# Kernel tuning notes

Measured on AMD Instinct MI355X. Metric: run time of the kernel, lower is better.

The kernel has to match this reference:

```python
import jax, jax.numpy as jnp
import numpy as np

K = 20          # neighbour_num
EMB = 512       # emb_dims
EPS = 1e-12     # guards sqrt grad at self-neighbor zero distance


def setup_inputs() -> dict:
    key = jax.random.key(0)
    ks = jax.random.split(key, 6)
    B, D, N = 8, 3, 4096
    C_in = 2 * D + K  # 26 = 6 + neighbour_num
    def xavier(k, o, c):
        return jax.random.normal(k, (o, c), jnp.float32) * jnp.sqrt(2.0 / (o + c))
    return {
        "x":  jax.random.normal(ks[0], (B, D, N), jnp.float32),
        "w1": xavier(ks[1], 64, C_in),
        "w2": xavier(ks[2], 64, 64),
        "w3": xavier(ks[3], 128, 64),
        "w4": xavier(ks[4], 256, 128),
        "w5": xavier(ks[5], EMB, 512),
    }


def _graph_feature(x):
    # x: (B, D, N). Returns (B, 2D+K, N, K).
    B, D, N = x.shape
    xt = jnp.swapaxes(x, 1, 2)                      # (B, N, D)
    sq = jnp.sum(x * x, axis=1)                     # (B, N)
    # pairwise = -||xi - xj||^2 ; topk picks nearest neighbors (incl. self)
    pair = 2.0 * jnp.einsum('bdn,bdm->bnm', x, x) - sq[:, :, None] - sq[:, None, :]
    idx = jax.lax.top_k(pair, K)[1]                 # (B, N, K) int32
    nbr = xt[jnp.arange(B)[:, None, None], idx]     # (B, N, K, D) gather
    xc = jnp.broadcast_to(xt[:, :, None, :], (B, N, K, D))
    dist = jnp.sqrt(jnp.sum((nbr - xc) ** 2, axis=-1) + EPS)   # (B, N, K)
    distr = jnp.broadcast_to(dist[:, :, None, :], (B, N, K, K))
    feat = jnp.concatenate([xc, nbr, distr], axis=-1)          # (B, N, K, 2D+K)
    return jnp.transpose(feat, (0, 3, 1, 2))        # (B, 2D+K, N, K)


def _conv1x1(h, w):
    # h: (B, C, N, K), w: (O, C)  -> (B, O, N, K)
    return jnp.einsum('bcnk,oc->bonk', h, w)


def reference(x, w1, w2, w3, w4, w5):
    h = _graph_feature(x)                           # (B, 26, N, K)
    h = jax.nn.relu(_conv1x1(h, w1)); x1 = h.max(axis=-1)   # (B, 64, N)
    h = jax.nn.relu(_conv1x1(h, w2)); x2 = h.max(axis=-1)   # (B, 64, N)
    h = jax.nn.relu(_conv1x1(h, w3)); x3 = h.max(axis=-1)   # (B, 128, N)
    h = jax.nn.relu(_conv1x1(h, w4)); x4 = h.max(axis=-1)   # (B, 256, N)
    cat = jnp.concatenate([x1, x2, x3, x4], axis=1)          # (B, 512, N)
    out = jax.nn.relu(jnp.einsum('bcn,oc->bon', cat, w5))    # (B, EMB, N)
    return out
```

## Files before the change

### kernel.cpp

```cpp
#include <hip/hip_runtime.h>
#include <cstdint>
#include <cstddef>

#define NB   8
#define NPTS 4096
#define KNN  20
#define P    4
#define QPW  4
#define WPB  8

typedef __attribute__((ext_vector_type(8))) short    short8;
typedef __attribute__((ext_vector_type(4))) float    floatx4;

__device__ __forceinline__ uint16_t f2bf(float f) {
    uint32_t u = __float_as_uint(f);
    uint32_t r = (u + 0x7FFFu + ((u >> 16) & 1u)) >> 16;
    return (uint16_t)r;
}

__device__ __forceinline__ uint32_t cvtpk_bf16(float lo, float hi) {
    uint32_t r;
    asm("v_cvt_pk_bf16_f32 %0, %1, %2" : "=v"(r) : "v"(lo), "v"(hi));
    return r;
}

#define NEGINF __int_as_float((int)0xFF800000)

__device__ __forceinline__ float rfl_f32(float v) {
    return __uint_as_float((uint32_t)__builtin_amdgcn_readfirstlane(__float_as_uint(v)));
}

template <int CTRL>
__device__ __forceinline__ float dpp_maxf(float v) {
    int o = __builtin_amdgcn_update_dpp(__float_as_int(v), __float_as_int(v),
                                        CTRL, 0xF, 0xF, false);
    return fmaxf(v, __int_as_float(o));
}
__device__ __forceinline__ float wave_max_f32(float v) {
    v = dpp_maxf<0x111>(v);
    v = dpp_maxf<0x112>(v);
    v = dpp_maxf<0x114>(v);
    v = dpp_maxf<0x118>(v);
    v = dpp_maxf<0x142>(v);
    v = dpp_maxf<0x143>(v);
    return __int_as_float(__builtin_amdgcn_readlane(__float_as_int(v), 63));
}

__global__ __launch_bounds__(512, 6) void topk_kernel(
    const float* __restrict__ x,
    int*   __restrict__ idx_out,
    float* __restrict__ dist_out)
{
    const int t = threadIdx.x;
    const int wave = t >> 6, l = t & 63;
    const int b = blockIdx.y;

    __shared__ float xs[NPTS], ys[NPTS], zs[NPTS];
    {
        const float* xb = x + (size_t)b * 3 * NPTS;
        for (int i = t; i < NPTS; i += WPB * 64) {
            xs[i] = xb[i];
            ys[i] = xb[NPTS + i];
            zs[i] = xb[2 * NPTS + i];
        }
    }
    __syncthreads();

    const int nbase = (blockIdx.x * WPB + wave) * QPW;

    float xn0[QPW], xn1[QPW], xn2[QPW], sqn[QPW];
    float V0[QPW], V1[QPW], V2[QPW];
    int   J0[QPW], J1[QPW], J2[QPW];
    int   my_m[QPW];

    #pragma unroll
    for (int p = 0; p < QPW; ++p) {
        const int n = nbase + p;
        const float qx = xs[n], qy = ys[n], qz = zs[n];
        xn0[p] = rfl_f32(qx); xn1[p] = rfl_f32(qy); xn2[p] = rfl_f32(qz);
        sqn[p] = rfl_f32(fmaf(qz, qz, fmaf(qy, qy, qx * qx)));
        V0[p] = NEGINF; V1[p] = NEGINF; V2[p] = NEGINF;
        J0[p] = 0; J1[p] = 0; J2[p] = 0;
        my_m[p] = 0;
    }

    #pragma unroll 2
    for (int j = 0; j < 64; ++j) {
        const float px = xs[j * 64 + l], py = ys[j * 64 + l], pz = zs[j * 64 + l];
        const float sqm = fmaf(pz, pz, fmaf(py, py, px * px));
        #pragma unroll
        for (int p = 0; p < QPW; ++p) {
            const float dot = fmaf(xn2[p], pz, fmaf(xn1[p], py, xn0[p] * px));
            const float s = fmaf(2.0f, dot, -sqn[p]) - sqm;
            const bool c0 = s > V0[p], c1 = s > V1[p], c2 = s > V2[p];
            const float nV2 = __builtin_amdgcn_fmed3f(V1[p], V2[p], s);
            const float nV1 = __builtin_amdgcn_fmed3f(V0[p], V1[p], s);
            V0[p] = fmaxf(V0[p], s);
            V1[p] = nV1; V2[p] = nV2;
            const int tA = c1 ? J1[p] : j;
            J2[p] = c2 ? tA : J2[p];
            const int tB = c0 ? J0[p] : j;
            J1[p] = c1 ? tB : J1[p];
            J0[p] = c0 ? j : J0[p];
        }
    }

    for (int k = 0; k < KNN; ++k) {
        #pragma unroll
        for (int p = 0; p < QPW; ++p) {
            if (V0[p] == NEGINF) {
                unsigned long long cons = 0ull;
                for (int i = 0; i < k; ++i) {
                    const int mw = __builtin_amdgcn_readlane(my_m[p], i);
                    if ((mw & 63) == l) cons |= 1ull << (mw >> 6);
                }
                V1[p] = NEGINF; V2[p] = NEGINF;
                for (int j = 0; j < 64; ++j) {
                    const float px = xs[j * 64 + l], py = ys[j * 64 + l], pz = zs[j * 64 + l];
                    const float sqm = fmaf(pz, pz, fmaf(py, py, px * px));
                    const float dot = fmaf(xn2[p], pz, fmaf(xn1[p], py, xn0[p] * px));
                    float s = fmaf(2.0f, dot, -sqn[p]) - sqm;
                    if ((cons >> j) & 1ull) s = NEGINF;
                    const bool c0 = s > V0[p], c1 = s > V1[p], c2 = s > V2[p];
                    const float nV2 = __builtin_amdgcn_fmed3f(V1[p], V2[p], s);
                    const float nV1 = __builtin_amdgcn_fmed3f(V0[p], V1[p], s);
                    V0[p] = fmaxf(V0[p], s);
                    V1[p] = nV1; V2[p] = nV2;
                    const int tA = c1 ? J1[p] : j;
                    J2[p] = c2 ? tA : J2[p];
                    const int tB = c0 ? J0[p] : j;
                    J1[p] = c1 ? tB : J1[p];
                    J0[p] = c0 ? j : J0[p];
                }
            }
        }
        float wv[QPW];
        #pragma unroll
        for (int p = 0; p < QPW; ++p) wv[p] = wave_max_f32(V0[p]);
        #pragma unroll
        for (int p = 0; p < QPW; ++p) {
            const unsigned long long own = __ballot(V0[p] == wv[p]);
            const int owner = (int)__builtin_ctzll(own);
            const int jwin  = __builtin_amdgcn_readlane(J0[p], owner);
            const int m     = jwin * 64 + owner;
            if (l == k) my_m[p] = m;
            if (l == owner) {
                V0[p] = V1[p]; V1[p] = V2[p]; V2[p] = NEGINF;
                J0[p] = J1[p]; J1[p] = J2[p];
            }
        }
    }

    #pragma unroll
    for (int p = 0; p < QPW; ++p) {
        if (l < KNN) {
            const int n = nbase + p;
            const int m = my_m[p];
            const float d0 = xs[m] - xn0[p], d1 = ys[m] - xn1[p], d2 = zs[m] - xn2[p];
            const float dist = sqrtf(((d0 * d0 + d1 * d1) + d2 * d2) + 1e-12f);
            const size_t base = ((size_t)b * NPTS + n) * KNN + l;
            idx_out[base]  = m;
            dist_out[base] = dist;
        }
    }
}

__global__ __launch_bounds__(256) void prep_all(
    const float* __restrict__ w1, const float* __restrict__ w2,
    const float* __restrict__ w3, const float* __restrict__ w4,
    const float* __restrict__ w5,
    uint16_t* __restrict__ wf1, uint16_t* __restrict__ wf2,
    uint16_t* __restrict__ wf3, uint16_t* __restrict__ wf4,
    uint16_t* __restrict__ w5b)
{
    int blk = blockIdx.x;
    const int t = threadIdx.x;
    if (blk < 1024) {
        const int i = blk * 256 + t;
        w5b[i] = f2bf(w5[i]);
        return;
    }
    blk -= 1024;
    const float* w; uint16_t* frag; int C, NT, KT, base;
    if (blk < 1)       { w = w1; frag = wf1; C = 26;  NT = 4;  KT = 1; base = blk; }
    else if (blk < 3)  { w = w2; frag = wf2; C = 64;  NT = 4;  KT = 2; base = blk - 1; }
    else if (blk < 7)  { w = w3; frag = wf3; C = 64;  NT = 8;  KT = 2; base = blk - 3; }
    else               { w = w4; frag = wf4; C = 128; NT = 16; KT = 4; base = blk - 7; }
    const int i = base * 256 + t;
    if (i >= NT * KT * 64) return;
    const int lane = i & 63;
    const int kt   = (i >> 6) % KT;
    const int nt   = (i >> 6) / KT;
    const int n    = nt * 16 + (lane & 15);
    const int c0   = kt * 32 + (lane >> 4) * 8;
    uint16_t o[8];
    #pragma unroll
    for (int j = 0; j < 8; ++j) {
        const int c = c0 + j;
        o[j] = (c < C) ? f2bf(w[(size_t)n * C + c]) : (uint16_t)0;
    }
    uint16_t* dst = frag + (size_t)i * 8;
    #pragma unroll
    for (int j = 0; j < 8; ++j) dst[j] = o[j];
}

template <int NT_TOT, int KT, int IN_STRIDE, int OUT_STRIDE>
__device__ __forceinline__ void mfma_layer(const uint16_t* __restrict__ in,
                                           uint16_t* __restrict__ out,
                                           const uint16_t* __restrict__ wf,
                                           int wave, int lane) {
    constexpr int NT_W = NT_TOT / 4;
    const int col = lane & 15, quad = lane >> 4;
    short8 bfrag[NT_W][KT];
    #pragma unroll
    for (int ni = 0; ni < NT_W; ++ni)
        #pragma unroll
        for (int k = 0; k < KT; ++k)
            bfrag[ni][k] = *(const short8*)(wf +
                ((size_t)((wave * NT_W + ni) * KT + k) * 64 + lane) * 8);
    #pragma unroll
    for (int mt = 0; mt < 5; ++mt) {
        short8 af[KT];
        #pragma unroll
        for (int k = 0; k < KT; ++k)
            af[k] = *(const short8*)(in + (mt * 16 + col) * IN_STRIDE + k * 32 + quad * 8);
        #pragma unroll
        for (int ni = 0; ni < NT_W; ++ni) {
            floatx4 acc = {0.f, 0.f, 0.f, 0.f};
            #pragma unroll
            for (int k = 0; k < KT; ++k)
                acc = __builtin_amdgcn_mfma_f32_16x16x32_bf16(af[k], bfrag[ni][k], acc, 0, 0, 0);
            const int nt = wave * NT_W + ni;
            const int rowb = mt * 16 + quad * 4;
            const uint32_t pk01 = cvtpk_bf16(fmaxf(acc[0], 0.f), fmaxf(acc[1], 0.f));
            const uint32_t pk23 = cvtpk_bf16(fmaxf(acc[2], 0.f), fmaxf(acc[3], 0.f));
            out[(rowb + 0) * OUT_STRIDE + nt * 16 + col] = (uint16_t)pk01;
            out[(rowb + 1) * OUT_STRIDE + nt * 16 + col] = (uint16_t)(pk01 >> 16);
            out[(rowb + 2) * OUT_STRIDE + nt * 16 + col] = (uint16_t)pk23;
            out[(rowb + 3) * OUT_STRIDE + nt * 16 + col] = (uint16_t)(pk23 >> 16);
        }
    }
}

template <int O, int STRIDE>
__device__ __forceinline__ void maxk(const uint16_t* __restrict__ h,
                                     uint16_t* __restrict__ cat_ws, int catoff,
                                     int t, int b, int n0) {
    constexpr int G = O / 8;
    if (t < P * G) {
        const int p = t / G, g = t % G;
        uint16_t mx[8];
        #pragma unroll
        for (int j = 0; j < 8; ++j) mx[j] = 0;
        for (int k = 0; k < KNN; ++k) {
            const uint16_t* row = h + (p * KNN + k) * STRIDE + g * 8;
            #pragma unroll
            for (int j = 0; j < 8; ++j) mx[j] = row[j] > mx[j] ? row[j] : mx[j];
        }
        uint16_t* dst = cat_ws + ((size_t)b * NPTS + n0 + p) * 512 + catoff + g * 8;
        *(short8*)dst = *(const short8*)mx;
    }
}

__global__ __launch_bounds__(256) void fused_mlp_mfma(
    const float* __restrict__ x,
    const int*   __restrict__ idx_ws,
    const float* __restrict__ dist_ws,
    const uint16_t* __restrict__ wf1,
    const uint16_t* __restrict__ wf2,
    const uint16_t* __restrict__ wf3,
    const uint16_t* __restrict__ wf4,
    uint16_t* __restrict__ cat_ws)
{
    const int n0 = blockIdx.x * P, b = blockIdx.y, t = threadIdx.x;
    const int wave = t >> 6, lane = t & 63;

    __shared__ __align__(16) uint16_t bufA[12800];
    __shared__ __align__(16) uint16_t bufB[10880];

    for (int i = t; i < 1600; i += 256) ((uint32_t*)bufA)[i] = 0;
    __syncthreads();
    {
        const float* xb = x + (size_t)b * 3 * NPTS;
        if (t < P * KNN) {
            const int p = t / KNN, k = t % KNN;
            const int n = n0 + p;
            const size_t base = ((size_t)b * NPTS + n) * KNN + k;
            const int   m = idx_ws[base];
            const float d = dist_ws[base];
            uint16_t* fr = bufA + t * 40;
            fr[0] = f2bf(xb[n]);        fr[1] = f2bf(xb[NPTS + n]);
            fr[2] = f2bf(xb[2 * NPTS + n]);
            fr[3] = f2bf(xb[m]);        fr[4] = f2bf(xb[NPTS + m]);
            fr[5] = f2bf(xb[2 * NPTS + m]);
            const uint16_t db = f2bf(d);
            #pragma unroll
            for (int j = 0; j < KNN; ++j) bufA[(p * KNN + j) * 40 + 6 + k] = db;
        }
    }
    __syncthreads();

    mfma_layer<4, 1, 40, 72>(bufA, bufB, wf1, wave, lane);
    __syncthreads();

    maxk<64, 72>(bufB, cat_ws, 0, t, b, n0);
    mfma_layer<4, 2, 72, 72>(bufB, bufA, wf2, wave, lane);
    __syncthreads();

    maxk<64, 72>(bufA, cat_ws, 64, t, b, n0);
    mfma_layer<8, 2, 72, 136>(bufA, bufB, wf3, wave, lane);
    __syncthreads();

    maxk<128, 136>(bufB, cat_ws, 128, t, b, n0);
    {
        float* slab = (float*)bufA + wave * 1600;
        const int col = lane & 15, quad = lane >> 4;
        #pragma unroll
        for (int ni = 0; ni < 4; ++ni) {
            const int nt = wave * 4 + ni;
            short8 bfrag[4];
            #pragma unroll
            for (int k = 0; k < 4; ++k)
                bfrag[k] = *(const short8*)(wf4 + ((size_t)(nt * 4 + k) * 64 + lane) * 8);
            #pragma unroll
            for (int mt = 0; mt < 5; ++mt) {
                floatx4 acc = {0.f, 0.f, 0.f, 0.f};
                #pragma unroll
                for (int k = 0; k < 4; ++k) {
                    const short8 af = *(const short8*)(bufB + (mt * 16 + col) * 136
                                                           + k * 32 + quad * 8);
                    acc = __builtin_amdgcn_mfma_f32_16x16x32_bf16(af, bfrag[k], acc, 0, 0, 0);
                }
                #pragma unroll
                for (int r = 0; r < 4; ++r)
                    slab[(mt * 16 + quad * 4 + r) * 20 + col] = fmaxf(acc[r], 0.f);
            }
            const int p = lane >> 4, grp = (lane >> 2) & 3, kq = lane & 3;
            floatx4 mx = {0.f, 0.f, 0.f, 0.f};
            #pragma unroll
            for (int i = 0; i < 5; ++i) {
                const floatx4 v = *(const floatx4*)&slab[(p * KNN + kq * 5 + i) * 20 + grp * 4];
                mx[0] = fmaxf(mx[0], v[0]); mx[1] = fmaxf(mx[1], v[1]);
                mx[2] = fmaxf(mx[2], v[2]); mx[3] = fmaxf(mx[3], v[3]);
            }
            #pragma unroll
            for (int r = 0; r < 4; ++r) {
                mx[r] = fmaxf(mx[r], __shfl_xor(mx[r], 1));
                mx[r] = fmaxf(mx[r], __shfl_xor(mx[r], 2));
            }
            if (kq == 0) {
                const uint32_t p01 = cvtpk_bf16(mx[0], mx[1]);
                const uint32_t p23 = cvtpk_bf16(mx[2], mx[3]);
                uint32_t* dst = (uint32_t*)(cat_ws + ((size_t)b * NPTS + n0 + p) * 512
                              + 256 + nt * 16 + grp * 4);
                dst[0] = p01; dst[1] = p23;
            }
        }
    }
}

__global__ __launch_bounds__(256) void final_gemm_mfma(
    const uint16_t* __restrict__ w5b,
    const uint16_t* __restrict__ cat,
    float* __restrict__ out)
{
    const int b  = blockIdx.z;
    const int o0 = blockIdx.y * 64;
    const int n0 = blockIdx.x * 128;
    const int t  = threadIdx.x;
    const int wave = t >> 6, lane = t & 63;
    const int col = lane & 15, quad = lane >> 4;

    __shared__ __align__(16) uint16_t As[64 * 72];
    __shared__ __align__(16) uint16_t Bs[128 * 72];

    floatx4 acc[8];
    #pragma unroll
    for (int i = 0; i < 8; ++i) acc[i] = (floatx4){0.f, 0.f, 0.f, 0.f};

    const size_t arow_base = (size_t)o0 * 512;
    const size_t brow_base = ((size_t)b * NPTS + n0) * 512;

    for (int kc = 0; kc < 512; kc += 64) {
        #pragma unroll
        for (int i = 0; i < 2; ++i) {
            const int idx = t + i * 256;
            const int row = idx >> 3;
            const int k8  = (idx & 7) * 8;
            *(short8*)&As[row * 72 + k8] =
                *(const short8*)&w5b[arow_base + (size_t)row * 512 + kc + k8];
        }
        #pragma unroll
        for (int i = 0; i < 4; ++i) {
            const int idx = t + i * 256;
            const int row = idx >> 3;
            const int k8  = (idx & 7) * 8;
            *(short8*)&Bs[row * 72 + k8] =
                *(const short8*)&cat[brow_base + (size_t)row * 512 + kc + k8];
        }
        __syncthreads();
        #pragma unroll
        for (int kt = 0; kt < 2; ++kt) {
            const short8 af = *(const short8*)&As[(wave * 16 + col) * 72 + kt * 32 + quad * 8];
            #pragma unroll
            for (int ns = 0; ns < 8; ++ns) {
                const short8 bf = *(const short8*)&Bs[(ns * 16 + col) * 72 + kt * 32 + quad * 8];
                acc[ns] = __builtin_amdgcn_mfma_f32_16x16x32_bf16(af, bf, acc[ns], 0, 0, 0);
            }
        }
        __syncthreads();
    }

    #pragma unroll
    for (int ns = 0; ns < 8; ++ns) {
        #pragma unroll
        for (int r = 0; r < 4; ++r) {
            out[((size_t)b * 512 + o0 + wave * 16 + quad * 4 + r) * NPTS
                + n0 + ns * 16 + col] = fmaxf(acc[ns][r], 0.f);
        }
    }
}

extern "C" void kernel_launch(void* const* d_in, const int* in_sizes, int n_in,
                              void* d_out, int out_size, void* d_ws, size_t ws_size,
                              hipStream_t stream) {
    const float* x  = (const float*)d_in[0];
    const float* w1 = (const float*)d_in[1];
    const float* w2 = (const float*)d_in[2];
    const float* w3 = (const float*)d_in[3];
    const float* w4 = (const float*)d_in[4];
    const float* w5 = (const float*)d_in[5];
    float* out = (float*)d_out;

    char* ws = (char*)d_ws;
    int*      idx_ws  = (int*)ws;
    float*    dist_ws = (float*)(ws + 2621440);
    uint16_t* cat_ws  = (uint16_t*)(ws + 5242880);
    uint16_t* w5b     = (uint16_t*)(ws + 38797312);
    uint16_t* wf1     = (uint16_t*)(ws + 72351744);
    uint16_t* wf2     = (uint16_t*)(ws + 72351744 + 4096);
    uint16_t* wf3     = (uint16_t*)(ws + 72351744 + 4096 + 8192);
    uint16_t* wf4     = (uint16_t*)(ws + 72351744 + 4096 + 8192 + 16384);

    prep_all<<<dim3(1024 + 23), 256, 0, stream>>>(w1, w2, w3, w4, w5,
                                                  wf1, wf2, wf3, wf4, w5b);

    topk_kernel<<<dim3(NPTS / (WPB * QPW), NB), WPB * 64, 0, stream>>>(x, idx_ws, dist_ws);
    fused_mlp_mfma<<<dim3(NPTS / P, NB), 256, 0, stream>>>(
        x, idx_ws, dist_ws, wf1, wf2, wf3, wf4, cat_ws);
    final_gemm_mfma<<<dim3(NPTS / 128, 512 / 64, NB), 256, 0, stream>>>(w5b, cat_ws, out);
}
```

Before: 359.7 us.

## Precompute packed xyz+norm in prep and read top-k points from global memory

The prep kernel now writes a packed float4 (x, y, z, squared norm) per point into workspace, reusing the cat buffer region before it is filled. The top-k kernel drops its 48KB shared-memory staging and reads the packed points straight from global memory (L2/L1 cached), using 256-thread blocks. It also keeps a per-lane consumed bitmask instead of rebuilding it from readlanes on every refill, and reorders the loops so each query's selection runs to completion. This removes the shared-memory load and barrier and the sqm recomputation, which should help occupancy, but every inner iteration now issues a global vector load instead of an LDS read.

```diff
diff --git a/kernel.cpp b/kernel.cpp
--- a/kernel.cpp
+++ b/kernel.cpp
@@ -7,7 +7,6 @@
 #define KNN  20
 #define P    4
 #define QPW  4
-#define WPB  8
 
 typedef __attribute__((ext_vector_type(8))) short    short8;
 typedef __attribute__((ext_vector_type(4))) float    floatx4;
@@ -25,10 +24,6 @@
 }
 
 #define NEGINF __int_as_float((int)0xFF800000)
-
-__device__ __forceinline__ float rfl_f32(float v) {
-    return __uint_as_float((uint32_t)__builtin_amdgcn_readfirstlane(__float_as_uint(v)));
-}
 
 template <int CTRL>
 __device__ __forceinline__ float dpp_maxf(float v) {
@@ -46,52 +41,40 @@
     return __int_as_float(__builtin_amdgcn_readlane(__float_as_int(v), 63));
 }
 
-__global__ __launch_bounds__(512, 6) void topk_kernel(
-    const float* __restrict__ x,
+__global__ __launch_bounds__(256) void topk_kernel(
+    const float4* __restrict__ xyzs,
     int*   __restrict__ idx_out,
     float* __restrict__ dist_out)
 {
     const int t = threadIdx.x;
     const int wave = t >> 6, l = t & 63;
+    const int nbase = (blockIdx.x * 4 + wave) * QPW;
     const int b = blockIdx.y;
-
-    __shared__ float xs[NPTS], ys[NPTS], zs[NPTS];
-    {
-        const float* xb = x + (size_t)b * 3 * NPTS;
-        for (int i = t; i < NPTS; i += WPB * 64) {
-            xs[i] = xb[i];
-            ys[i] = xb[NPTS + i];
-            zs[i] = xb[2 * NPTS + i];
-        }
-    }
-    __syncthreads();
-
-    const int nbase = (blockIdx.x * WPB + wave) * QPW;
+    const float4* xq = xyzs + (size_t)b * NPTS;
 
     float xn0[QPW], xn1[QPW], xn2[QPW], sqn[QPW];
     float V0[QPW], V1[QPW], V2[QPW];
     int   J0[QPW], J1[QPW], J2[QPW];
+    unsigned long long consumed[QPW];
     int   my_m[QPW];
 
     #pragma unroll
     for (int p = 0; p < QPW; ++p) {
-        const int n = nbase + p;
-        const float qx = xs[n], qy = ys[n], qz = zs[n];
-        xn0[p] = rfl_f32(qx); xn1[p] = rfl_f32(qy); xn2[p] = rfl_f32(qz);
-        sqn[p] = rfl_f32(fmaf(qz, qz, fmaf(qy, qy, qx * qx)));
+        const float4 pn = xq[nbase + p];
+        xn0[p] = pn.x; xn1[p] = pn.y; xn2[p] = pn.z; sqn[p] = pn.w;
         V0[p] = NEGINF; V1[p] = NEGINF; V2[p] = NEGINF;
         J0[p] = 0; J1[p] = 0; J2[p] = 0;
+        consumed[p] = 0ull;
         my_m[p] = 0;
     }
 
-    #pragma unroll 2
+    #pragma unroll 4
     for (int j = 0; j < 64; ++j) {
-        const float px = xs[j * 64 + l], py = ys[j * 64 + l], pz = zs[j * 64 + l];
-        const float sqm = fmaf(pz, pz, fmaf(py, py, px * px));
+        const float4 pm = xq[j * 64 + l];
         #pragma unroll
         for (int p = 0; p < QPW; ++p) {
-            const float dot = fmaf(xn2[p], pz, fmaf(xn1[p], py, xn0[p] * px));
-            const float s = fmaf(2.0f, dot, -sqn[p]) - sqm;
+            const float dot = fmaf(xn2[p], pm.z, fmaf(xn1[p], pm.y, xn0[p] * pm.x));
+            const float s = fmaf(2.0f, dot, -sqn[p]) - pm.w;
             const bool c0 = s > V0[p], c1 = s > V1[p], c2 = s > V2[p];
             const float nV2 = __builtin_amdgcn_fmed3f(V1[p], V2[p], s);
             const float nV1 = __builtin_amdgcn_fmed3f(V0[p], V1[p], s);
@@ -105,22 +88,16 @@
         }
     }
 
-    for (int k = 0; k < KNN; ++k) {
-        #pragma unroll
-        for (int p = 0; p < QPW; ++p) {
+    #pragma unroll
+    for (int p = 0; p < QPW; ++p) {
+        for (int k = 0; k < KNN; ++k) {
             if (V0[p] == NEGINF) {
-                unsigned long long cons = 0ull;
-                for (int i = 0; i < k; ++i) {
-                    const int mw = __builtin_amdgcn_readlane(my_m[p], i);
-                    if ((mw & 63) == l) cons |= 1ull << (mw >> 6);
-                }
                 V1[p] = NEGINF; V2[p] = NEGINF;
                 for (int j = 0; j < 64; ++j) {
-                    const float px = xs[j * 64 + l], py = ys[j * 64 + l], pz = zs[j * 64 + l];
-                    const float sqm = fmaf(pz, pz, fmaf(py, py, px * px));
-                    const float dot = fmaf(xn2[p], pz, fmaf(xn1[p], py, xn0[p] * px));
-                    float s = fmaf(2.0f, dot, -sqn[p]) - sqm;
-                    if ((cons >> j) & 1ull) s = NEGINF;
+                    const float4 pm = xq[j * 64 + l];
+                    const float dot = fmaf(xn2[p], pm.z, fmaf(xn1[p], pm.y, xn0[p] * pm.x));
+                    float s = fmaf(2.0f, dot, -sqn[p]) - pm.w;
+                    if ((consumed[p] >> j) & 1ull) s = NEGINF;
                     const bool c0 = s > V0[p], c1 = s > V1[p], c2 = s > V2[p];
                     const float nV2 = __builtin_amdgcn_fmed3f(V1[p], V2[p], s);
                     const float nV1 = __builtin_amdgcn_fmed3f(V0[p], V1[p], s);
@@ -133,18 +110,14 @@
                     J0[p] = c0 ? j : J0[p];
                 }
             }
-        }
-        float wv[QPW];
-        #pragma unroll
-        for (int p = 0; p < QPW; ++p) wv[p] = wave_max_f32(V0[p]);
-        #pragma unroll
-        for (int p = 0; p < QPW; ++p) {
-            const unsigned long long own = __ballot(V0[p] == wv[p]);
+            const float w = wave_max_f32(V0[p]);
+            const unsigned long long own = __ballot(V0[p] == w);
             const int owner = (int)__builtin_ctzll(own);
             const int jwin  = __builtin_amdgcn_readlane(J0[p], owner);
             const int m     = jwin * 64 + owner;
             if (l == k) my_m[p] = m;
             if (l == owner) {
+                consumed[p] |= 1ull << J0[p];
                 V0[p] = V1[p]; V1[p] = V2[p]; V2[p] = NEGINF;
                 J0[p] = J1[p]; J1[p] = J2[p];
             }
@@ -155,23 +128,25 @@
     for (int p = 0; p < QPW; ++p) {
         if (l < KNN) {
             const int n = nbase + p;
-            const int m = my_m[p];
-            const float d0 = xs[m] - xn0[p], d1 = ys[m] - xn1[p], d2 = zs[m] - xn2[p];
+            const float4 pm = xq[my_m[p]];
+            const float d0 = pm.x - xn0[p], d1 = pm.y - xn1[p], d2 = pm.z - xn2[p];
             const float dist = sqrtf(((d0 * d0 + d1 * d1) + d2 * d2) + 1e-12f);
             const size_t base = ((size_t)b * NPTS + n) * KNN + l;
-            idx_out[base]  = m;
+            idx_out[base]  = my_m[p];
             dist_out[base] = dist;
         }
     }
 }
 
 __global__ __launch_bounds__(256) void prep_all(
+    const float* __restrict__ x,
     const float* __restrict__ w1, const float* __restrict__ w2,
     const float* __restrict__ w3, const float* __restrict__ w4,
     const float* __restrict__ w5,
     uint16_t* __restrict__ wf1, uint16_t* __restrict__ wf2,
     uint16_t* __restrict__ wf3, uint16_t* __restrict__ wf4,
-    uint16_t* __restrict__ w5b)
+    uint16_t* __restrict__ w5b,
+    float4* __restrict__ xyzs)
 {
     int blk = blockIdx.x;
     const int t = threadIdx.x;
@@ -181,6 +156,19 @@
         return;
     }
     blk -= 1024;
+    if (blk >= 23) {
+        const int i = (blk - 23) * 256 + t;
+        if (i < NB * NPTS) {
+            const int b = i / NPTS, n = i - b * NPTS;
+            const float* xb = x + (size_t)b * 3 * NPTS;
+            const float x0 = xb[n], x1 = xb[NPTS + n], x2 = xb[2 * NPTS + n];
+            float4 v;
+            v.x = x0; v.y = x1; v.z = x2;
+            v.w = fmaf(x2, x2, fmaf(x1, x1, x0 * x0));
+            xyzs[i] = v;
+        }
+        return;
+    }
     const float* w; uint16_t* frag; int C, NT, KT, base;
     if (blk < 1)       { w = w1; frag = wf1; C = 26;  NT = 4;  KT = 1; base = blk; }
     else if (blk < 3)  { w = w2; frag = wf2; C = 64;  NT = 4;  KT = 2; base = blk - 1; }
@@ -436,16 +424,17 @@
     int*      idx_ws  = (int*)ws;
     float*    dist_ws = (float*)(ws + 2621440);
     uint16_t* cat_ws  = (uint16_t*)(ws + 5242880);
+    float4*   xyzs    = (float4*)(ws + 5242880);
     uint16_t* w5b     = (uint16_t*)(ws + 38797312);
     uint16_t* wf1     = (uint16_t*)(ws + 72351744);
     uint16_t* wf2     = (uint16_t*)(ws + 72351744 + 4096);
     uint16_t* wf3     = (uint16_t*)(ws + 72351744 + 4096 + 8192);
     uint16_t* wf4     = (uint16_t*)(ws + 72351744 + 4096 + 8192 + 16384);
 
-    prep_all<<<dim3(1024 + 23), 256, 0, stream>>>(w1, w2, w3, w4, w5,
-                                                  wf1, wf2, wf3, wf4, w5b);
-
-    topk_kernel<<<dim3(NPTS / (WPB * QPW), NB), WPB * 64, 0, stream>>>(x, idx_ws, dist_ws);
+    prep_all<<<dim3(1024 + 23 + 128), 256, 0, stream>>>(
+        x, w1, w2, w3, w4, w5, wf1, wf2, wf3, wf4, w5b, xyzs);
+
+    topk_kernel<<<dim3(NPTS / (4 * QPW), NB), 256, 0, stream>>>(xyzs, idx_ws, dist_ws);
     fused_mlp_mfma<<<dim3(NPTS / P, NB), 256, 0, stream>>>(
         x, idx_ws, dist_ws, wf1, wf2, wf3, wf4, cat_ws);
     final_gemm_mfma<<<dim3(NPTS / 128, 512 / 64, NB), 256, 0, stream>>>(w5b, cat_ws, out);
```

Measured after the change: 353.5 us. About the same (-1.7%).
